# Performance work log

Measured on AMD Instinct MI355X. Metric: run time of the kernel, lower is better.

The kernel has to match this reference:

```python
import jax, jax.numpy as jnp
import numpy as np

H = 32  # rnn/encoder/residual hidden dim
NEG = -1e9


def gru(x, h0, Wih, Whh, bih, bhh):
    # x: (B,T,D), h0: (B,H); torch GRU gate order [r,z,n]
    xp = jnp.swapaxes(x @ Wih.T + bih, 0, 1)  # (T,B,3H)

    def step(h, xt):
        gh = h @ Whh.T + bhh
        xr, xz, xn = jnp.split(xt, 3, axis=-1)
        hr, hz, hn = jnp.split(gh, 3, axis=-1)
        r = jax.nn.sigmoid(xr + hr)
        z = jax.nn.sigmoid(xz + hz)
        n = jnp.tanh(xn + r * hn)
        h_new = (1.0 - z) * n + z * h
        return h_new, h_new

    hT, ys = jax.lax.scan(step, h0, xp)
    return jnp.swapaxes(ys, 0, 1), hT  # (B,T,H), (B,H)


def setup_inputs():
    key = jax.random.key(0)
    ks = jax.random.split(key, 30)
    B, T = 2048, 128
    def lin(k, o, i):
        return jax.random.normal(k, (o, i), jnp.float32) / np.sqrt(i)
    inp = {}
    inp['obs'] = jax.random.normal(ks[0], (B, T, 15), jnp.float32)
    inp['rnn_state'] = jax.random.normal(ks[1], (1, B, 3 * H), jnp.float32)
    inp['enc_air_W'] = lin(ks[2], H, 7); inp['enc_air_b'] = jnp.zeros((H,), jnp.float32)
    inp['enc_m_W'] = lin(ks[3], H, 4); inp['enc_m_b'] = jnp.zeros((H,), jnp.float32)
    inp['air_Wih'] = lin(ks[4], 3 * H, H); inp['air_Whh'] = lin(ks[5], 3 * H, H)
    inp['air_bih'] = jnp.zeros((3 * H,), jnp.float32); inp['air_bhh'] = jnp.zeros((3 * H,), jnp.float32)
    inp['m_Wih'] = lin(ks[6], 3 * H, H); inp['m_Whh'] = lin(ks[7], 3 * H, H)
    inp['m_bih'] = jnp.zeros((3 * H,), jnp.float32); inp['m_bhh'] = jnp.zeros((3 * H,), jnp.float32)
    inp['attn_in_w'] = lin(ks[8], 3 * H, H); inp['attn_in_b'] = jnp.zeros((3 * H,), jnp.float32)
    inp['attn_out_w'] = lin(ks[9], H, H); inp['attn_out_b'] = jnp.zeros((H,), jnp.float32)
    inp['mlp_W0'] = lin(ks[10], 256, 2 * H); inp['mlp_b0'] = jnp.zeros((256,), jnp.float32)
    inp['mlp_W1'] = lin(ks[11], 256, 256); inp['mlp_b1'] = jnp.zeros((256,), jnp.float32)
    inp['out_W'] = lin(ks[12], 1, 256); inp['out_b'] = jnp.zeros((1,), jnp.float32)
    return inp


def reference(obs, rnn_state, enc_air_W, enc_air_b, enc_m_W, enc_m_b,
              air_Wih, air_Whh, air_bih, air_bhh,
              m_Wih, m_Whh, m_bih, m_bhh,
              attn_in_w, attn_in_b, attn_out_w, attn_out_b,
              mlp_W0, mlp_b0, mlp_W1, mlp_b1, out_W, out_b):
    B, T, _ = obs.shape
    h_air0 = rnn_state[0, :, :H]                       # (B,H)
    h_m0 = rnn_state[0, :, H:].reshape(2 * B, H)       # faithful reshape (1,B,64)->(1,2B,32)

    # aircraft branch
    air_emb = obs[..., 8:] @ enc_air_W.T + enc_air_b   # (B,T,H)
    air_feat, next_h_air = gru(air_emb, h_air0, air_Wih, air_Whh, air_bih, air_bhh)

    # missile branch: concat missiles along batch dim
    m_raw = jnp.concatenate([obs[..., 0:4], obs[..., 4:8]], axis=0)  # (2B,T,4)
    m_emb = m_raw @ enc_m_W.T + enc_m_b
    m_feat, next_h_m = gru(m_emb, h_m0, m_Wih, m_Whh, m_bih, m_bhh)
    m1_feat, m2_feat = m_feat[:B], m_feat[B:]

    # inactive-missile mask from raw obs
    obs_flat = obs.reshape(-1, 15)
    inact = jnp.array([1.0, 0.0, 1.0, 0.0], jnp.float32)
    mask = jnp.stack([
        jnp.all(jnp.isclose(obs_flat[:, 0:4], inact), axis=-1),
        jnp.all(jnp.isclose(obs_flat[:, 4:8], inact), axis=-1),
    ], axis=1)                                          # (N,2) True = masked

    N = B * T
    air_flat = air_feat.reshape(N, H)
    m1_flat = m1_feat.reshape(N, H)
    m2_flat = m2_feat.reshape(N, H)

    # 2-head attention, q len 1, kv len 2
    Wq, Wk, Wv = jnp.split(attn_in_w, 3, axis=0)
    bq, bk, bv = jnp.split(attn_in_b, 3, axis=0)
    nh, hd = 2, H // 2
    qh = (air_flat @ Wq.T + bq).reshape(N, nh, hd)
    kv = jnp.stack([m1_flat, m2_flat], axis=1)          # (N,2,H)
    kh = (kv @ Wk.T + bk).reshape(N, 2, nh, hd)
    vh = (kv @ Wv.T + bv).reshape(N, 2, nh, hd)
    scores = jnp.einsum('nhd,nkhd->nhk', qh, kh) / np.sqrt(hd)
    scores = scores + jnp.where(mask[:, None, :], NEG, 0.0)
    w = jax.nn.softmax(scores, axis=-1)
    ctx = jnp.einsum('nhk,nkhd->nhd', w, vh).reshape(N, H)
    attn = ctx @ attn_out_w.T + attn_out_b
    attn = jnp.where(jnp.all(mask, axis=-1, keepdims=True), 0.0, attn)  # torch nan_to_num(all-masked)

    fusion = jnp.concatenate([air_flat, attn], axis=-1)  # (N,2H)
    h1 = jax.nn.leaky_relu(fusion @ mlp_W0.T + mlp_b0, 0.01)
    h2 = jax.nn.leaky_relu(h1 @ mlp_W1.T + mlp_b1, 0.01)
    val = h2 @ out_W.T + out_b                           # (N,1)

    next_h = jnp.concatenate([next_h_air, next_h_m.reshape(B, 2 * H)], axis=-1)[None]  # (1,B,96)
    return val, next_h
```

## Files before the change

### kernel.cpp

```cpp
#include <hip/hip_runtime.h>
#include <hip/hip_bf16.h>

#define BB 2048
#define TT 128
#define NN (BB*TT)
#define NVAL NN

#define OFF_BCA   768u
#define OFF_BCM   1632u
#define OFF_W0P   2048u
#define OFF_W1P   10240u
#define OFF_WQKV  43008u
#define OFF_WO    44544u
#define OFF_WH2A  45568u
#define OFF_WH2M  47104u
#define OFF_WC2A  48640u
#define OFF_WC2M  49024u
#define OFF_AIRF  83968u
#define OFF_MF    4278272u
#define OFF_MASK  12666880u

typedef __attribute__((ext_vector_type(8))) short short8;
typedef __attribute__((ext_vector_type(4))) float f32x4;
typedef _Float16 h2 __attribute__((ext_vector_type(2)));

__device__ __forceinline__ unsigned short f2bf(float f) {
    unsigned u = __builtin_bit_cast(unsigned, f);
    u += 0x7FFFu + ((u >> 16) & 1u);
    return (unsigned short)(u >> 16);
}
__device__ __forceinline__ unsigned f2h(float f) {
    _Float16 h = (_Float16)f;
    return (unsigned)__builtin_bit_cast(unsigned short, h);
}
__device__ __forceinline__ unsigned pkh2(float a, float b) {
    return (f2h(b) << 16) | f2h(a);
}
__device__ __forceinline__ float dot2(unsigned w, unsigned x, float acc) {
    return __builtin_amdgcn_fdot2(__builtin_bit_cast(h2, w),
                                  __builtin_bit_cast(h2, x), acc, false);
}
__device__ __forceinline__ float fast_rcp(float x) {
    return __builtin_amdgcn_rcpf(x);
}

__global__ __launch_bounds__(256) void prep_kernel(
    const float* __restrict__ enc_air_W, const float* __restrict__ enc_air_b,
    const float* __restrict__ enc_m_W,   const float* __restrict__ enc_m_b,
    const float* __restrict__ air_Wih,   const float* __restrict__ air_bih,
    const float* __restrict__ m_Wih,     const float* __restrict__ m_bih,
    const float* __restrict__ air_Whh,   const float* __restrict__ m_Whh,
    const float* __restrict__ W0,        const float* __restrict__ W1,
    const float* __restrict__ attn_in_w, const float* __restrict__ attn_out_w,
    float* __restrict__ ws)
{
    int b = blockIdx.x, t = threadIdx.x;
    if (b == 0) {
        if (t < 96) {
            float bacc = air_bih[t];
            for (int k = 0; k < 32; k++) bacc += air_Wih[t*32+k] * enc_air_b[k];
            ws[OFF_BCA + t] = bacc;
            float bacc2 = m_bih[t];
            for (int k = 0; k < 32; k++) bacc2 += m_Wih[t*32+k] * enc_m_b[k];
            ws[OFF_BCM + t] = bacc2;
        }
    } else if (b <= 32) {
        unsigned short* w1p = (unsigned short*)(ws + OFF_W1P);
        int base = ((b-1)*256 + t);
        int lane = base & 63;
        int ctf  = base >> 6;
        int ct   = ctf & 15, s = ctf >> 4;
        int col = lane & 15, quad = lane >> 4;
        int k0 = s*32 + quad*8;
        int o  = ct*16 + col;
        #pragma unroll
        for (int j = 0; j < 8; j++)
            w1p[base*8 + j] = f2bf(W1[o*256 + k0 + j]);
    } else if (b <= 40) {
        unsigned short* w0p = (unsigned short*)(ws + OFF_W0P);
        int base = ((b-33)*256 + t);
        int lane = base & 63;
        int ctf  = base >> 6;
        int ct   = ctf & 15, s = ctf >> 4;
        int col = lane & 15, quad = lane >> 4;
        int k0 = s*32 + quad*8;
        int o  = ct*16 + col;
        #pragma unroll
        for (int j = 0; j < 8; j++)
            w0p[base*8 + j] = f2bf(W0[o*64 + k0 + j]);
    } else if (b == 41) {
        unsigned short* wqkv = (unsigned short*)(ws + OFF_WQKV);
        unsigned short* wop  = (unsigned short*)(ws + OFF_WO);
        for (int slot = t; slot < 512; slot += 256) {
            if (slot < 384) {
                int ct = slot >> 6, lane = slot & 63;
                int col = lane & 15, quad = lane >> 4;
                int o = ct*16 + col;
                #pragma unroll
                for (int j = 0; j < 8; j++)
                    wqkv[slot*8 + j] = f2bf(attn_in_w[o*32 + quad*8 + j]);
            } else {
                int s2 = slot - 384;
                int ct = s2 >> 6, lane = s2 & 63;
                int col = lane & 15, quad = lane >> 4;
                #pragma unroll
                for (int j = 0; j < 8; j++)
                    wop[s2*8 + j] = f2bf(attn_out_w[(ct*16+col)*32 + quad*8 + j]);
            }
        }
    } else if (b == 42) {
        unsigned* wa = (unsigned*)(ws + OFF_WH2A);
        unsigned* wm = (unsigned*)(ws + OFF_WH2M);
        for (int s = t; s < 3072; s += 256) {
            int s2 = (s < 1536) ? s : s - 1536;
            const float* W = (s < 1536) ? air_Whh : m_Whh;
            unsigned* dst = (s < 1536) ? wa : wm;
            int o = s2 >> 4, j = s2 & 15;
            dst[s2] = pkh2(W[o*32 + 2*j], W[o*32 + 2*j + 1]);
        }
    } else {
        unsigned* wa = (unsigned*)(ws + OFF_WC2A);
        unsigned* wm = (unsigned*)(ws + OFF_WC2M);
        for (int s = t; s < 768; s += 256) {
            int s2 = (s < 384) ? s : s - 384;
            bool is_air = (s < 384);
            unsigned* dst = is_air ? wa : wm;
            int o = s2 >> 2, j = s2 & 3;
            int ni  = is_air ? 7 : 4;
            float c0 = 0.f, c1 = 0.f;
            int i0 = 2*j, i1 = 2*j + 1;
            if (i0 < ni)
                for (int k = 0; k < 32; k++)
                    c0 += (is_air ? air_Wih[o*32+k]*enc_air_W[k*7+i0]
                                  : m_Wih[o*32+k]*enc_m_W[k*4+i0]);
            if (i1 < ni)
                for (int k = 0; k < 32; k++)
                    c1 += (is_air ? air_Wih[o*32+k]*enc_air_W[k*7+i1]
                                  : m_Wih[o*32+k]*enc_m_W[k*4+i1]);
            dst[s2] = pkh2(c0, c1);
        }
    }
}

template<int NI, int NP, bool DO_MASK>
__device__ void gru_row(const float* __restrict__ in_base,
                        const unsigned* __restrict__ wc2,
                        const float* __restrict__ bc,
                        const unsigned* __restrict__ wh2,
                        const float* __restrict__ bhh,
                        float h0,
                        unsigned short* __restrict__ feat_out,
                        float* __restrict__ hT_out,
                        float* __restrict__ mask_out,
                        int lane, int half)
{
    unsigned whr[16], whz[16], whn[16];
    #pragma unroll
    for (int j = 0; j < 16; j++) {
        whr[j] = wh2[lane*16 + j];
        whz[j] = wh2[(32+lane)*16 + j];
        whn[j] = wh2[(64+lane)*16 + j];
    }
    unsigned cr2[NP], cz2[NP], cn2[NP];
    #pragma unroll
    for (int j = 0; j < NP; j++) {
        cr2[j] = wc2[lane*4 + j];
        cz2[j] = wc2[(32+lane)*4 + j];
        cn2[j] = wc2[(64+lane)*4 + j];
    }
    const float bcr = bc[lane], bcz = bc[32+lane], bcn = bc[64+lane];
    const float bhr = bhh[lane], bhz = bhh[32+lane], bhn = bhh[64+lane];

    float h = h0;
    for (int t = 0; t < TT; t++) {
        float xin = (lane < NI) ? in_base[t*15 + lane] : 0.f;

        bool ok = true;
        if (DO_MASK) {
            bool pred = true;
            if (lane < 4) {
                const float c   = ((lane & 1) == 0) ? 1.f : 0.f;
                const float thr = ((lane & 1) == 0) ? 1.00001e-5f : 1e-8f;
                pred = fabsf(xin - c) <= thr;
            }
            unsigned long long ball = __ballot(pred);
            ok = (((ball >> (half*32)) & 0xFull) == 0xFull);
        }

        unsigned x16 = f2h(xin);
        unsigned xnb = (unsigned)__shfl_xor((int)x16, 1, 32);
        unsigned xpk = (xnb << 16) | x16;

        float ar = bcr, az = bcz, an = bcn;
        #pragma unroll
        for (int j = 0; j < NP; j++) {
            unsigned px = (unsigned)__shfl((int)xpk, 2*j, 32);
            ar = dot2(cr2[j], px, ar);
            az = dot2(cz2[j], px, az);
            an = dot2(cn2[j], px, an);
        }

        unsigned h16 = f2h(h);
        unsigned hnb = (unsigned)__shfl_xor((int)h16, 1, 32);
        unsigned hpk = (hnb << 16) | h16;

        float hr0 = bhr, hz0 = bhz, hn0 = bhn;
        float hr1 = 0.f, hz1 = 0.f, hn1 = 0.f;
        #pragma unroll
        for (int j = 0; j < 8; j++) {
            unsigned pa = (unsigned)__shfl((int)hpk, 2*j, 32);
            unsigned pb = (unsigned)__shfl((int)hpk, 2*(j+8), 32);
            hr0 = dot2(whr[j],   pa, hr0);
            hr1 = dot2(whr[j+8], pb, hr1);
            hz0 = dot2(whz[j],   pa, hz0);
            hz1 = dot2(whz[j+8], pb, hz1);
            hn0 = dot2(whn[j],   pa, hn0);
            hn1 = dot2(whn[j+8], pb, hn1);
        }
        float hr = hr0 + hr1, hz = hz0 + hz1, hn = hn0 + hn1;

        float r = fast_rcp(1.f + __expf(-(ar + hr)));
        float z = fast_rcp(1.f + __expf(-(az + hz)));
        float pre = an + r*hn;
        float e2 = __expf(2.f*pre);
        float n = 1.f - 2.f*fast_rcp(e2 + 1.f);
        h = n + z*(h - n);

        unsigned bf = f2bf(h);
        unsigned nb = (unsigned)__shfl_xor((int)bf, 1, 32);
        if ((lane & 1) == 0)
            *(unsigned*)(feat_out + t*32 + lane) = (nb << 16) | bf;

        if (DO_MASK && lane == 0) mask_out[t*2] = ok ? 1.f : 0.f;
    }
    *hT_out = h;
}

__global__ __launch_bounds__(256) void gru_kernel(
    const float* __restrict__ obs, const float* __restrict__ rnn,
    const float* __restrict__ ws,
    const float* __restrict__ air_bhh, const float* __restrict__ m_bhh,
    unsigned short* __restrict__ air_feat, unsigned short* __restrict__ m_feat,
    float* __restrict__ mask_f, float* __restrict__ nh_out)
{
    int lane = threadIdx.x & 31;
    int half = (threadIdx.x >> 5) & 1;
    int r = blockIdx.x*8 + (threadIdx.x >> 5);
    if (r < BB) {
        const float* in_base = obs + r*(TT*15) + 8;
        float h0 = rnn[r*96 + lane];
        gru_row<7,4,false>(in_base,
                         (const unsigned*)(ws + OFF_WC2A), ws + OFF_BCA,
                         (const unsigned*)(ws + OFF_WH2A), air_bhh, h0,
                         air_feat + (size_t)r*TT*32,
                         nh_out + r*96 + lane, nullptr, lane, half);
    } else {
        int i = r - BB;
        int b = (i < BB) ? i : i - BB;
        int slot = (i < BB) ? 0 : 1;
        const float* in_base = obs + b*(TT*15) + slot*4;
        float h0 = rnn[(i >> 1)*96 + 32 + (i & 1)*32 + lane];
        gru_row<4,2,true>(in_base,
                        (const unsigned*)(ws + OFF_WC2M), ws + OFF_BCM,
                        (const unsigned*)(ws + OFF_WH2M), m_bhh, h0,
                        m_feat + (size_t)i*TT*32,
                        nh_out + (i >> 1)*96 + 32 + (i & 1)*32 + lane,
                        mask_f + (size_t)(b*TT)*2 + slot, lane, half);
    }
}

__global__ __launch_bounds__(256) void fused_kernel(
    const unsigned short* __restrict__ air_feat, const unsigned short* __restrict__ m_feat,
    const float* __restrict__ mask_f,
    const unsigned short* __restrict__ wqkv, const float* __restrict__ attn_in_b,
    const unsigned short* __restrict__ wop,  const float* __restrict__ attn_out_b,
    const unsigned short* __restrict__ w0p, const float* __restrict__ b0,
    const unsigned short* __restrict__ w1p, const float* __restrict__ b1,
    const float* __restrict__ outW, const float* __restrict__ outb,
    float* __restrict__ val)
{
    __shared__ unsigned short A1[64*72];
    __shared__ unsigned short U[64*264];
    __shared__ float MS[128];
    __shared__ float PS[4][64];

    unsigned short* AM = U;
    unsigned short* CT = U + 64*72;
    unsigned short* A2 = U;

    const int tid  = threadIdx.x;
    const int lane = tid & 63;
    const int strip = tid >> 6;
    const int col  = lane & 15;
    const int quad = lane >> 4;
    const size_t n0 = (size_t)blockIdx.x * 64;

    short8 wqf[2], wkf[2], wvf[2], wof[2];
    #pragma unroll
    for (int ct = 0; ct < 2; ct++) {
        wqf[ct] = *(const short8*)(wqkv + ((0+ct)*64 + lane)*8);
        wkf[ct] = *(const short8*)(wqkv + ((2+ct)*64 + lane)*8);
        wvf[ct] = *(const short8*)(wqkv + ((4+ct)*64 + lane)*8);
        wof[ct] = *(const short8*)(wop + (ct*64 + lane)*8);
    }

    {
        int row = tid >> 2, c0 = (tid & 3)*8;
        short8 va  = *(const short8*)(air_feat + (n0 + row)*32 + c0);
        *(short8*)&A1[row*72 + c0] = va;
        short8 vm1 = *(const short8*)(m_feat + (n0 + row)*32 + c0);
        *(short8*)&AM[row*72 + c0] = vm1;
        short8 vm2 = *(const short8*)(m_feat + ((size_t)NN + n0 + row)*32 + c0);
        *(short8*)&AM[row*72 + 32 + c0] = vm2;
        if (tid < 128) MS[tid] = mask_f[n0*2 + tid];
    }
    __syncthreads();

    {
        short8 a_air = *(const short8*)&A1[(strip*16 + col)*72 + quad*8];
        short8 a_m1  = *(const short8*)&AM[(strip*16 + col)*72 + quad*8];
        short8 a_m2  = *(const short8*)&AM[(strip*16 + col)*72 + 32 + quad*8];

        f32x4 q[2], k1[2], k2[2], v1[2], v2[2], ao[2];
        #pragma unroll
        for (int ct = 0; ct < 2; ct++) {
            f32x4 z = (f32x4){0.f,0.f,0.f,0.f};
            q[ct]  = __builtin_amdgcn_mfma_f32_16x16x32_bf16(a_air, wqf[ct], z, 0,0,0);
            k1[ct] = __builtin_amdgcn_mfma_f32_16x16x32_bf16(a_m1,  wkf[ct], z, 0,0,0);
            k2[ct] = __builtin_amdgcn_mfma_f32_16x16x32_bf16(a_m2,  wkf[ct], z, 0,0,0);
            v1[ct] = __builtin_amdgcn_mfma_f32_16x16x32_bf16(a_m1,  wvf[ct], z, 0,0,0);
            v2[ct] = __builtin_amdgcn_mfma_f32_16x16x32_bf16(a_m2,  wvf[ct], z, 0,0,0);
        }
        float bqr[2], bkr[2], bvr[2];
        #pragma unroll
        for (int ct = 0; ct < 2; ct++) {
            bqr[ct] = attn_in_b[ct*16 + col];
            bkr[ct] = attn_in_b[32 + ct*16 + col];
            bvr[ct] = attn_in_b[64 + ct*16 + col];
        }
        float p1s[2][4], p2s[2][4];
        #pragma unroll
        for (int ct = 0; ct < 2; ct++) {
            #pragma unroll
            for (int reg = 0; reg < 4; reg++) {
                float qq = q[ct][reg] + bqr[ct];
                float p1 = qq * (k1[ct][reg] + bkr[ct]);
                float p2 = qq * (k2[ct][reg] + bkr[ct]);
                #pragma unroll
                for (int m = 1; m < 16; m <<= 1) {
                    p1 += __shfl_xor(p1, m, 64);
                    p2 += __shfl_xor(p2, m, 64);
                }
                p1s[ct][reg] = p1; p2s[ct][reg] = p2;
            }
        }
        float bothm[4];
        #pragma unroll
        for (int reg = 0; reg < 4; reg++) {
            int rloc = strip*16 + quad*4 + reg;
            float m0v = MS[rloc*2], m1v = MS[rloc*2 + 1];
            bothm[reg] = (m0v > 0.5f && m1v > 0.5f) ? 1.f : 0.f;
            #pragma unroll
            for (int ct = 0; ct < 2; ct++) {
                float s1 = p1s[ct][reg]*0.25f + (m0v > 0.5f ? -1e9f : 0.f);
                float s2 = p2s[ct][reg]*0.25f + (m1v > 0.5f ? -1e9f : 0.f);
                float mx = fmaxf(s1, s2);
                float e1 = __expf(s1 - mx), e2 = __expf(s2 - mx);
                float inv = fast_rcp(e1 + e2);
                float ctxv = ((v1[ct][reg] + bvr[ct])*e1 +
                              (v2[ct][reg] + bvr[ct])*e2) * inv;
                CT[rloc*40 + ct*16 + col] = f2bf(ctxv);
            }
        }
        short8 a_ctx = *(const short8*)&CT[(strip*16 + col)*40 + quad*8];
        #pragma unroll
        for (int ct = 0; ct < 2; ct++) {
            f32x4 z = (f32x4){0.f,0.f,0.f,0.f};
            ao[ct] = __builtin_amdgcn_mfma_f32_16x16x32_bf16(a_ctx, wof[ct], z, 0,0,0);
        }
        float bor[2] = { attn_out_b[col], attn_out_b[16 + col] };
        #pragma unroll
        for (int reg = 0; reg < 4; reg++) {
            int rloc = strip*16 + quad*4 + reg;
            #pragma unroll
            for (int ct = 0; ct < 2; ct++) {
                float av = ao[ct][reg] + bor[ct];
                av = (bothm[reg] > 0.5f) ? 0.f : av;
                A1[rloc*72 + 32 + ct*16 + col] = f2bf(av);
            }
        }
    }
    __syncthreads();

    float b0r[4], b1r[4], owr[4];
    #pragma unroll
    for (int c = 0; c < 4; c++) {
        int ct = strip*4 + c;
        b0r[c] = b0[ct*16 + col];
        b1r[c] = b1[ct*16 + col];
        owr[c] = outW[ct*16 + col];
    }
    const float outb0 = outb[0];

    f32x4 acc1[4][4];
    #pragma unroll
    for (int s = 0; s < 4; s++)
        #pragma unroll
        for (int c = 0; c < 4; c++) acc1[s][c] = (f32x4){0.f,0.f,0.f,0.f};
    {
        short8 bfr[4], nbfr[4];
        #pragma unroll
        for (int c = 0; c < 4; c++)
            bfr[c] = *(const short8*)(w0p + ((0*16 + strip*4 + c)*64 + lane)*8);
        #pragma unroll
        for (int ks = 0; ks < 2; ks++) {
            if (ks < 1) {
                #pragma unroll
                for (int c = 0; c < 4; c++)
                    nbfr[c] = *(const short8*)(w0p + (((ks+1)*16 + strip*4 + c)*64 + lane)*8);
            }
            short8 a[4];
            #pragma unroll
            for (int s = 0; s < 4; s++)
                a[s] = *(const short8*)&A1[(s*16 + col)*72 + ks*32 + quad*8];
            #pragma unroll
            for (int c = 0; c < 4; c++)
                #pragma unroll
                for (int s = 0; s < 4; s++)
                    acc1[s][c] = __builtin_amdgcn_mfma_f32_16x16x32_bf16(a[s], bfr[c], acc1[s][c], 0, 0, 0);
            #pragma unroll
            for (int c = 0; c < 4; c++) bfr[c] = nbfr[c];
        }
    }
    __syncthreads();
    #pragma unroll
    for (int s = 0; s < 4; s++) {
        #pragma unroll
        for (int c = 0; c < 4; c++) {
            int ct = strip*4 + c;
            #pragma unroll
            for (int reg = 0; reg < 4; reg++) {
                float h = acc1[s][c][reg] + b0r[c];
                h = (h > 0.f) ? h : 0.01f*h;
                A2[(s*16 + quad*4 + reg)*264 + ct*16 + col] = f2bf(h);
            }
        }
    }
    __syncthreads();

    f32x4 acc2[4][4];
    #pragma unroll
    for (int s = 0; s < 4; s++)
        #pragma unroll
        for (int c = 0; c < 4; c++) acc2[s][c] = (f32x4){0.f,0.f,0.f,0.f};
    {
        short8 bfr[4], nbfr[4];
        #pragma unroll
        for (int c = 0; c < 4; c++)
            bfr[c] = *(const short8*)(w1p + ((0*16 + strip*4 + c)*64 + lane)*8);
        #pragma unroll
        for (int ks = 0; ks < 8; ks++) {
            if (ks < 7) {
                #pragma unroll
                for (int c = 0; c < 4; c++)
                    nbfr[c] = *(const short8*)(w1p + (((ks+1)*16 + strip*4 + c)*64 + lane)*8);
            }
            short8 a[4];
            #pragma unroll
            for (int s = 0; s < 4; s++)
                a[s] = *(const short8*)&A2[(s*16 + col)*264 + ks*32 + quad*8];
            #pragma unroll
            for (int c = 0; c < 4; c++)
                #pragma unroll
                for (int s = 0; s < 4; s++)
                    acc2[s][c] = __builtin_amdgcn_mfma_f32_16x16x32_bf16(a[s], bfr[c], acc2[s][c], 0, 0, 0);
            #pragma unroll
            for (int c = 0; c < 4; c++) bfr[c] = nbfr[c];
        }
    }

    #pragma unroll
    for (int s = 0; s < 4; s++) {
        float pv[4];
        #pragma unroll
        for (int reg = 0; reg < 4; reg++) pv[reg] = 0.f;
        #pragma unroll
        for (int c = 0; c < 4; c++) {
            #pragma unroll
            for (int reg = 0; reg < 4; reg++) {
                float h = acc2[s][c][reg] + b1r[c];
                h = (h > 0.f) ? h : 0.01f*h;
                pv[reg] += h*owr[c];
            }
        }
        #pragma unroll
        for (int reg = 0; reg < 4; reg++) {
            #pragma unroll
            for (int m = 1; m < 16; m <<= 1)
                pv[reg] += __shfl_xor(pv[reg], m, 64);
            if (col == 0) PS[strip][s*16 + quad*4 + reg] = pv[reg];
        }
    }
    __syncthreads();
    if (tid < 64)
        val[n0 + tid] = PS[0][tid] + PS[1][tid] + PS[2][tid] + PS[3][tid] + outb0;
}

extern "C" void kernel_launch(void* const* d_in, const int* in_sizes, int n_in,
                              void* d_out, int out_size, void* d_ws, size_t ws_size,
                              hipStream_t stream) {
    const float* obs        = (const float*)d_in[0];
    const float* rnn        = (const float*)d_in[1];
    const float* enc_air_W  = (const float*)d_in[2];
    const float* enc_air_b  = (const float*)d_in[3];
    const float* enc_m_W    = (const float*)d_in[4];
    const float* enc_m_b    = (const float*)d_in[5];
    const float* air_Wih    = (const float*)d_in[6];
    const float* air_Whh    = (const float*)d_in[7];
    const float* air_bih    = (const float*)d_in[8];
    const float* air_bhh    = (const float*)d_in[9];
    const float* m_Wih      = (const float*)d_in[10];
    const float* m_Whh      = (const float*)d_in[11];
    const float* m_bih      = (const float*)d_in[12];
    const float* m_bhh      = (const float*)d_in[13];
    const float* attn_in_w  = (const float*)d_in[14];
    const float* attn_in_b  = (const float*)d_in[15];
    const float* attn_out_w = (const float*)d_in[16];
    const float* attn_out_b = (const float*)d_in[17];
    const float* mlp_W0     = (const float*)d_in[18];
    const float* mlp_b0     = (const float*)d_in[19];
    const float* mlp_W1     = (const float*)d_in[20];
    const float* mlp_b1     = (const float*)d_in[21];
    const float* out_W      = (const float*)d_in[22];
    const float* out_b      = (const float*)d_in[23];

    float* ws  = (float*)d_ws;
    float* out = (float*)d_out;

    prep_kernel<<<44, 256, 0, stream>>>(enc_air_W, enc_air_b, enc_m_W, enc_m_b,
                                        air_Wih, air_bih, m_Wih, m_bih,
                                        air_Whh, m_Whh,
                                        mlp_W0, mlp_W1, attn_in_w, attn_out_w, ws);

    gru_kernel<<<768, 256, 0, stream>>>(obs, rnn, ws, air_bhh, m_bhh,
                                        (unsigned short*)(ws + OFF_AIRF),
                                        (unsigned short*)(ws + OFF_MF),
                                        ws + OFF_MASK, out + NVAL);

    fused_kernel<<<NN/64, 256, 0, stream>>>((const unsigned short*)(ws + OFF_AIRF),
                                            (const unsigned short*)(ws + OFF_MF),
                                            ws + OFF_MASK,
                                            (const unsigned short*)(ws + OFF_WQKV), attn_in_b,
                                            (const unsigned short*)(ws + OFF_WO),   attn_out_b,
                                            (const unsigned short*)(ws + OFF_W0P), mlp_b0,
                                            (const unsigned short*)(ws + OFF_W1P), mlp_b1,
                                            out_W, out_b, out);
}
```

Measured before the change: 324.8 us.

## Run GRU recurrence as batched 16-row MFMA tiles instead of per-row dot2 shuffles

The GRU step moves from one sequence per 32 lanes, which uses fdot2 with cross-lane shuffles, to 16 sequences per wavefront using 16x16x32 f16 MFMA for both the input and hidden projections. Prep now packs the weights into MFMA fragment layout and folds the biases into an extra constant-one input column. The next timestep's inputs are prefetched one step ahead. The launch shrinks to 384 single-wave blocks, so far fewer wavefronts run the serial 128-step loop, which risks lower latency hiding per CU.

```diff
diff --git a/kernel.cpp b/kernel.cpp
--- a/kernel.cpp
+++ b/kernel.cpp
@@ -6,23 +6,24 @@
 #define NN (BB*TT)
 #define NVAL NN
 
-#define OFF_BCA   768u
-#define OFF_BCM   1632u
 #define OFF_W0P   2048u
 #define OFF_W1P   10240u
 #define OFF_WQKV  43008u
 #define OFF_WO    44544u
-#define OFF_WH2A  45568u
-#define OFF_WH2M  47104u
-#define OFF_WC2A  48640u
-#define OFF_WC2M  49024u
+#define OFF_PWHA  49792u
+#define OFF_PWHM  51328u
+#define OFF_PWCA  52864u
+#define OFF_PWCM  54400u
+#define OFF_BHNA  55936u
+#define OFF_BHNM  55968u
 #define OFF_AIRF  83968u
 #define OFF_MF    4278272u
 #define OFF_MASK  12666880u
 
 typedef __attribute__((ext_vector_type(8))) short short8;
 typedef __attribute__((ext_vector_type(4))) float f32x4;
-typedef _Float16 h2 __attribute__((ext_vector_type(2)));
+typedef _Float16 f16x8 __attribute__((ext_vector_type(8)));
+typedef unsigned u32x4 __attribute__((ext_vector_type(4)));
 
 __device__ __forceinline__ unsigned short f2bf(float f) {
     unsigned u = __builtin_bit_cast(unsigned, f);
@@ -36,12 +37,16 @@
 __device__ __forceinline__ unsigned pkh2(float a, float b) {
     return (f2h(b) << 16) | f2h(a);
 }
-__device__ __forceinline__ float dot2(unsigned w, unsigned x, float acc) {
-    return __builtin_amdgcn_fdot2(__builtin_bit_cast(h2, w),
-                                  __builtin_bit_cast(h2, x), acc, false);
-}
 __device__ __forceinline__ float fast_rcp(float x) {
     return __builtin_amdgcn_rcpf(x);
+}
+__device__ __forceinline__ unsigned cvt_pk_bf16(float a, float b) {
+    unsigned r;
+    asm("v_cvt_pk_bf16_f32 %0, %1, %2" : "=v"(r) : "v"(a), "v"(b));
+    return r;
+}
+__device__ __forceinline__ f32x4 mfma16f(f16x8 a, f16x8 b, f32x4 c) {
+    return __builtin_amdgcn_mfma_f32_16x16x32_f16(a, b, c, 0, 0, 0);
 }
 
 __global__ __launch_bounds__(256) void prep_kernel(
@@ -50,20 +55,13 @@
     const float* __restrict__ air_Wih,   const float* __restrict__ air_bih,
     const float* __restrict__ m_Wih,     const float* __restrict__ m_bih,
     const float* __restrict__ air_Whh,   const float* __restrict__ m_Whh,
+    const float* __restrict__ air_bhh,   const float* __restrict__ m_bhh,
     const float* __restrict__ W0,        const float* __restrict__ W1,
     const float* __restrict__ attn_in_w, const float* __restrict__ attn_out_w,
     float* __restrict__ ws)
 {
     int b = blockIdx.x, t = threadIdx.x;
     if (b == 0) {
-        if (t < 96) {
-            float bacc = air_bih[t];
-            for (int k = 0; k < 32; k++) bacc += air_Wih[t*32+k] * enc_air_b[k];
-            ws[OFF_BCA + t] = bacc;
-            float bacc2 = m_bih[t];
-            for (int k = 0; k < 32; k++) bacc2 += m_Wih[t*32+k] * enc_m_b[k];
-            ws[OFF_BCM + t] = bacc2;
-        }
     } else if (b <= 32) {
         unsigned short* w1p = (unsigned short*)(ws + OFF_W1P);
         int base = ((b-1)*256 + t);
@@ -109,164 +107,197 @@
             }
         }
     } else if (b == 42) {
-        unsigned* wa = (unsigned*)(ws + OFF_WH2A);
-        unsigned* wm = (unsigned*)(ws + OFF_WH2M);
+        unsigned* pa = (unsigned*)(ws + OFF_PWHA);
+        unsigned* pm = (unsigned*)(ws + OFF_PWHM);
         for (int s = t; s < 3072; s += 256) {
             int s2 = (s < 1536) ? s : s - 1536;
             const float* W = (s < 1536) ? air_Whh : m_Whh;
-            unsigned* dst = (s < 1536) ? wa : wm;
-            int o = s2 >> 4, j = s2 & 15;
-            dst[s2] = pkh2(W[o*32 + 2*j], W[o*32 + 2*j + 1]);
+            unsigned* dst = (s < 1536) ? pa : pm;
+            int tile = s2 >> 8;
+            int l    = (s2 >> 2) & 63;
+            int d    = s2 & 3;
+            int gate = tile >> 1, hfp = tile & 1;
+            int rr = l & 15;
+            int f  = (rr >> 2)*8 + hfp*4 + (rr & 3);
+            int k  = (l >> 4)*8 + d*2;
+            int row = gate*32 + f;
+            dst[s2] = pkh2(W[row*32 + k], W[row*32 + k + 1]);
         }
     } else {
-        unsigned* wa = (unsigned*)(ws + OFF_WC2A);
-        unsigned* wm = (unsigned*)(ws + OFF_WC2M);
-        for (int s = t; s < 768; s += 256) {
-            int s2 = (s < 384) ? s : s - 384;
-            bool is_air = (s < 384);
-            unsigned* dst = is_air ? wa : wm;
-            int o = s2 >> 2, j = s2 & 3;
-            int ni  = is_air ? 7 : 4;
-            float c0 = 0.f, c1 = 0.f;
-            int i0 = 2*j, i1 = 2*j + 1;
-            if (i0 < ni)
-                for (int k = 0; k < 32; k++)
-                    c0 += (is_air ? air_Wih[o*32+k]*enc_air_W[k*7+i0]
-                                  : m_Wih[o*32+k]*enc_m_W[k*4+i0]);
-            if (i1 < ni)
-                for (int k = 0; k < 32; k++)
-                    c1 += (is_air ? air_Wih[o*32+k]*enc_air_W[k*7+i1]
-                                  : m_Wih[o*32+k]*enc_m_W[k*4+i1]);
-            dst[s2] = pkh2(c0, c1);
-        }
-    }
-}
-
-template<int NI, int NP, bool DO_MASK>
-__device__ void gru_row(const float* __restrict__ in_base,
-                        const unsigned* __restrict__ wc2,
-                        const float* __restrict__ bc,
-                        const unsigned* __restrict__ wh2,
-                        const float* __restrict__ bhh,
-                        float h0,
-                        unsigned short* __restrict__ feat_out,
-                        float* __restrict__ hT_out,
-                        float* __restrict__ mask_out,
-                        int lane, int half)
-{
-    unsigned whr[16], whz[16], whn[16];
-    #pragma unroll
-    for (int j = 0; j < 16; j++) {
-        whr[j] = wh2[lane*16 + j];
-        whz[j] = wh2[(32+lane)*16 + j];
-        whn[j] = wh2[(64+lane)*16 + j];
-    }
-    unsigned cr2[NP], cz2[NP], cn2[NP];
-    #pragma unroll
-    for (int j = 0; j < NP; j++) {
-        cr2[j] = wc2[lane*4 + j];
-        cz2[j] = wc2[(32+lane)*4 + j];
-        cn2[j] = wc2[(64+lane)*4 + j];
-    }
-    const float bcr = bc[lane], bcz = bc[32+lane], bcn = bc[64+lane];
-    const float bhr = bhh[lane], bhz = bhh[32+lane], bhn = bhh[64+lane];
-
-    float h = h0;
-    for (int t = 0; t < TT; t++) {
-        float xin = (lane < NI) ? in_base[t*15 + lane] : 0.f;
-
-        bool ok = true;
-        if (DO_MASK) {
-            bool pred = true;
-            if (lane < 4) {
-                const float c   = ((lane & 1) == 0) ? 1.f : 0.f;
-                const float thr = ((lane & 1) == 0) ? 1.00001e-5f : 1e-8f;
-                pred = fabsf(xin - c) <= thr;
-            }
-            unsigned long long ball = __ballot(pred);
-            ok = (((ball >> (half*32)) & 0xFull) == 0xFull);
-        }
-
-        unsigned x16 = f2h(xin);
-        unsigned xnb = (unsigned)__shfl_xor((int)x16, 1, 32);
-        unsigned xpk = (xnb << 16) | x16;
-
-        float ar = bcr, az = bcz, an = bcn;
-        #pragma unroll
-        for (int j = 0; j < NP; j++) {
-            unsigned px = (unsigned)__shfl((int)xpk, 2*j, 32);
-            ar = dot2(cr2[j], px, ar);
-            az = dot2(cz2[j], px, az);
-            an = dot2(cn2[j], px, an);
-        }
-
-        unsigned h16 = f2h(h);
-        unsigned hnb = (unsigned)__shfl_xor((int)h16, 1, 32);
-        unsigned hpk = (hnb << 16) | h16;
-
-        float hr0 = bhr, hz0 = bhz, hn0 = bhn;
-        float hr1 = 0.f, hz1 = 0.f, hn1 = 0.f;
-        #pragma unroll
-        for (int j = 0; j < 8; j++) {
-            unsigned pa = (unsigned)__shfl((int)hpk, 2*j, 32);
-            unsigned pb = (unsigned)__shfl((int)hpk, 2*(j+8), 32);
-            hr0 = dot2(whr[j],   pa, hr0);
-            hr1 = dot2(whr[j+8], pb, hr1);
-            hz0 = dot2(whz[j],   pa, hz0);
-            hz1 = dot2(whz[j+8], pb, hz1);
-            hn0 = dot2(whn[j],   pa, hn0);
-            hn1 = dot2(whn[j+8], pb, hn1);
-        }
-        float hr = hr0 + hr1, hz = hz0 + hz1, hn = hn0 + hn1;
-
-        float r = fast_rcp(1.f + __expf(-(ar + hr)));
-        float z = fast_rcp(1.f + __expf(-(az + hz)));
-        float pre = an + r*hn;
-        float e2 = __expf(2.f*pre);
-        float n = 1.f - 2.f*fast_rcp(e2 + 1.f);
-        h = n + z*(h - n);
-
-        unsigned bf = f2bf(h);
-        unsigned nb = (unsigned)__shfl_xor((int)bf, 1, 32);
-        if ((lane & 1) == 0)
-            *(unsigned*)(feat_out + t*32 + lane) = (nb << 16) | bf;
-
-        if (DO_MASK && lane == 0) mask_out[t*2] = ok ? 1.f : 0.f;
-    }
-    *hT_out = h;
-}
-
-__global__ __launch_bounds__(256) void gru_kernel(
+        unsigned* pa = (unsigned*)(ws + OFF_PWCA);
+        unsigned* pm = (unsigned*)(ws + OFF_PWCM);
+        for (int s = t; s < 3072; s += 256) {
+            bool isA = (s < 1536);
+            int s2 = isA ? s : s - 1536;
+            unsigned* dst = isA ? pa : pm;
+            int tile = s2 >> 8, l = (s2 >> 2) & 63, d = s2 & 3;
+            int gate = tile >> 1, hfp = tile & 1;
+            int rr = l & 15;
+            int f = (rr >> 2)*8 + hfp*4 + (rr & 3);
+            int o = gate*32 + f;
+            int kb = (l >> 4)*8 + d*2;
+            int ni = isA ? 7 : 4;
+            float v[2];
+            #pragma unroll
+            for (int e = 0; e < 2; e++) {
+                int k = kb + e;
+                float acc = 0.f;
+                if (k < ni) {
+                    for (int m = 0; m < 32; m++)
+                        acc += isA ? air_Wih[o*32+m]*enc_air_W[m*7+k]
+                                   : m_Wih[o*32+m]*enc_m_W[m*4+k];
+                } else if (k == ni) {
+                    acc = isA ? air_bih[o] : m_bih[o];
+                    for (int m = 0; m < 32; m++)
+                        acc += isA ? air_Wih[o*32+m]*enc_air_b[m]
+                                   : m_Wih[o*32+m]*enc_m_b[m];
+                    if (gate < 2) acc += isA ? air_bhh[o] : m_bhh[o];
+                }
+                v[e] = acc;
+            }
+            dst[s2] = pkh2(v[0], v[1]);
+        }
+        if (t < 32) {
+            ws[OFF_BHNA + t] = air_bhh[64 + t];
+            ws[OFF_BHNM + t] = m_bhh[64 + t];
+        }
+    }
+}
+
+template<bool AIRT>
+__device__ __forceinline__ void gru_tile(
     const float* __restrict__ obs, const float* __restrict__ rnn,
     const float* __restrict__ ws,
-    const float* __restrict__ air_bhh, const float* __restrict__ m_bhh,
+    unsigned short* __restrict__ feat, float* __restrict__ mask_f,
+    float* __restrict__ nh_out, int tileIdx)
+{
+    const int lane = threadIdx.x & 63;
+    const int col = lane & 15, quad = lane >> 4;
+    const bool q0 = (quad == 0);
+
+    const unsigned* pw = (const unsigned*)(ws + (AIRT ? OFF_PWHA : OFF_PWHM));
+    const unsigned* pc = (const unsigned*)(ws + (AIRT ? OFF_PWCA : OFF_PWCM));
+    f16x8 whf[6], wcf[6];
+    #pragma unroll
+    for (int i6 = 0; i6 < 6; i6++) {
+        whf[i6] = __builtin_bit_cast(f16x8, *(const u32x4*)(pw + i6*256 + lane*4));
+        wcf[i6] = __builtin_bit_cast(f16x8, *(const u32x4*)(pc + i6*256 + lane*4));
+    }
+    const float* bhnp = ws + (AIRT ? OFF_BHNA : OFF_BHNM) + quad*8;
+    f32x4 bhn0 = *(const f32x4*)(bhnp);
+    f32x4 bhn1 = *(const f32x4*)(bhnp + 4);
+
+    int hbase, brow = 0, slot = 0;
+    size_t featOff;
+    const float* xptr;
+    if (AIRT) {
+        int r = tileIdx*16 + col;
+        hbase = r*96;
+        featOff = (size_t)r*(TT*32);
+        xptr = obs + (size_t)r*(TT*15) + 8;
+    } else {
+        int i = tileIdx*16 + col;
+        slot = (i >= BB) ? 1 : 0;
+        brow = i - slot*BB;
+        hbase = (i >> 1)*96 + 32 + (i & 1)*32;
+        featOff = (size_t)i*(TT*32);
+        xptr = obs + (size_t)brow*(TT*15) + slot*4;
+    }
+    unsigned short* featp = feat + featOff + quad*8;
+
+    f32x4 h0v = *(const f32x4*)(rnn + hbase + quad*8);
+    f32x4 h1v = *(const f32x4*)(rnn + hbase + quad*8 + 4);
+
+    constexpr int NI = AIRT ? 7 : 4;
+    float nx[NI];
+    #pragma unroll
+    for (int u = 0; u < NI; u++) nx[u] = xptr[u];
+
+    #pragma unroll 1
+    for (int t = 0; t < TT; t++) {
+        float cx[NI];
+        #pragma unroll
+        for (int u = 0; u < NI; u++) cx[u] = nx[u];
+        const int tn = (t < TT-1) ? (t+1)*15 : t*15;
+        #pragma unroll
+        for (int u = 0; u < NI; u++) nx[u] = xptr[tn + u];
+
+        if (!AIRT) {
+            bool ok = (fabsf(cx[0] - 1.f) <= 1.00001e-5f) &&
+                      (fabsf(cx[1])       <= 1e-8f) &&
+                      (fabsf(cx[2] - 1.f) <= 1.00001e-5f) &&
+                      (fabsf(cx[3])       <= 1e-8f);
+            if (q0) mask_f[((size_t)brow*TT + t)*2 + slot] = ok ? 1.f : 0.f;
+        }
+
+        unsigned xd0, xd1, xd2, xd3;
+        if (AIRT) {
+            xd0 = pkh2(cx[0], cx[1]); xd1 = pkh2(cx[2], cx[3]);
+            xd2 = pkh2(cx[4], cx[5]); xd3 = pkh2(cx[6], 1.0f);
+        } else {
+            xd0 = pkh2(cx[0], cx[1]); xd1 = pkh2(cx[2], cx[3]);
+            xd2 = 0x00003C00u;        xd3 = 0u;
+        }
+        u32x4 xdv;
+        xdv[0] = q0 ? xd0 : 0u; xdv[1] = q0 ? xd1 : 0u;
+        xdv[2] = q0 ? xd2 : 0u; xdv[3] = q0 ? xd3 : 0u;
+        f16x8 xf = __builtin_bit_cast(f16x8, xdv);
+
+        u32x4 hdv;
+        hdv[0] = pkh2(h0v[0], h0v[1]); hdv[1] = pkh2(h0v[2], h0v[3]);
+        hdv[2] = pkh2(h1v[0], h1v[1]); hdv[3] = pkh2(h1v[2], h1v[3]);
+        f16x8 hff = __builtin_bit_cast(f16x8, hdv);
+
+        const f32x4 z4 = {0.f, 0.f, 0.f, 0.f};
+        f32x4 aR0 = mfma16f(whf[0], hff, mfma16f(wcf[0], xf, z4));
+        f32x4 aR1 = mfma16f(whf[1], hff, mfma16f(wcf[1], xf, z4));
+        f32x4 aZ0 = mfma16f(whf[2], hff, mfma16f(wcf[2], xf, z4));
+        f32x4 aZ1 = mfma16f(whf[3], hff, mfma16f(wcf[3], xf, z4));
+        f32x4 aXN0 = mfma16f(wcf[4], xf, z4);
+        f32x4 aXN1 = mfma16f(wcf[5], xf, z4);
+        f32x4 aHN0 = mfma16f(whf[4], hff, z4);
+        f32x4 aHN1 = mfma16f(whf[5], hff, z4);
+
+        #pragma unroll
+        for (int s = 0; s < 4; s++) {
+            {
+                float r  = fast_rcp(1.f + __expf(-aR0[s]));
+                float z  = fast_rcp(1.f + __expf(-aZ0[s]));
+                float hn = aHN0[s] + bhn0[s];
+                float pre = aXN0[s] + r*hn;
+                float e2 = __expf(2.f*pre);
+                float n  = 1.f - 2.f*fast_rcp(e2 + 1.f);
+                h0v[s] = n + z*(h0v[s] - n);
+            }
+            {
+                float r  = fast_rcp(1.f + __expf(-aR1[s]));
+                float z  = fast_rcp(1.f + __expf(-aZ1[s]));
+                float hn = aHN1[s] + bhn1[s];
+                float pre = aXN1[s] + r*hn;
+                float e2 = __expf(2.f*pre);
+                float n  = 1.f - 2.f*fast_rcp(e2 + 1.f);
+                h1v[s] = n + z*(h1v[s] - n);
+            }
+        }
+
+        u32x4 fw;
+        fw[0] = cvt_pk_bf16(h0v[0], h0v[1]); fw[1] = cvt_pk_bf16(h0v[2], h0v[3]);
+        fw[2] = cvt_pk_bf16(h1v[0], h1v[1]); fw[3] = cvt_pk_bf16(h1v[2], h1v[3]);
+        *(u32x4*)(featp + (size_t)t*32) = fw;
+    }
+    *(f32x4*)(nh_out + hbase + quad*8)     = h0v;
+    *(f32x4*)(nh_out + hbase + quad*8 + 4) = h1v;
+}
+
+__global__ __launch_bounds__(64) void gru_kernel(
+    const float* __restrict__ obs, const float* __restrict__ rnn,
+    const float* __restrict__ ws,
     unsigned short* __restrict__ air_feat, unsigned short* __restrict__ m_feat,
     float* __restrict__ mask_f, float* __restrict__ nh_out)
 {
-    int lane = threadIdx.x & 31;
-    int half = (threadIdx.x >> 5) & 1;
-    int r = blockIdx.x*8 + (threadIdx.x >> 5);
-    if (r < BB) {
-        const float* in_base = obs + r*(TT*15) + 8;
-        float h0 = rnn[r*96 + lane];
-        gru_row<7,4,false>(in_base,
-                         (const unsigned*)(ws + OFF_WC2A), ws + OFF_BCA,
-                         (const unsigned*)(ws + OFF_WH2A), air_bhh, h0,
-                         air_feat + (size_t)r*TT*32,
-                         nh_out + r*96 + lane, nullptr, lane, half);
-    } else {
-        int i = r - BB;
-        int b = (i < BB) ? i : i - BB;
-        int slot = (i < BB) ? 0 : 1;
-        const float* in_base = obs + b*(TT*15) + slot*4;
-        float h0 = rnn[(i >> 1)*96 + 32 + (i & 1)*32 + lane];
-        gru_row<4,2,true>(in_base,
-                        (const unsigned*)(ws + OFF_WC2M), ws + OFF_BCM,
-                        (const unsigned*)(ws + OFF_WH2M), m_bhh, h0,
-                        m_feat + (size_t)i*TT*32,
-                        nh_out + (i >> 1)*96 + 32 + (i & 1)*32 + lane,
-                        mask_f + (size_t)(b*TT)*2 + slot, lane, half);
-    }
+    int g = blockIdx.x;
+    if (g < 128) gru_tile<true >(obs, rnn, ws, air_feat, mask_f, nh_out, g);
+    else         gru_tile<false>(obs, rnn, ws, m_feat,  mask_f, nh_out, g - 128);
 }
 
 __global__ __launch_bounds__(256) void fused_kernel(
@@ -539,13 +570,13 @@
 
     prep_kernel<<<44, 256, 0, stream>>>(enc_air_W, enc_air_b, enc_m_W, enc_m_b,
                                         air_Wih, air_bih, m_Wih, m_bih,
-                                        air_Whh, m_Whh,
+                                        air_Whh, m_Whh, air_bhh, m_bhh,
                                         mlp_W0, mlp_W1, attn_in_w, attn_out_w, ws);
 
-    gru_kernel<<<768, 256, 0, stream>>>(obs, rnn, ws, air_bhh, m_bhh,
-                                        (unsigned short*)(ws + OFF_AIRF),
-                                        (unsigned short*)(ws + OFF_MF),
-                                        ws + OFF_MASK, out + NVAL);
+    gru_kernel<<<384, 64, 0, stream>>>(obs, rnn, ws,
+                                       (unsigned short*)(ws + OFF_AIRF),
+                                       (unsigned short*)(ws + OFF_MF),
+                                       ws + OFF_MASK, out + NVAL);
 
     fused_kernel<<<NN/64, 256, 0, stream>>>((const unsigned short*)(ws + OFF_AIRF),
                                             (const unsigned short*)(ws + OFF_MF),
```

New measurement: 352.5 us. 8.5% more time.
